# Kernel tuning notes

Measured on AMD Instinct MI355X. Metric: run time of the kernel, lower is better.

The kernel has to match this reference:

```python
import jax, jax.numpy as jnp
import numpy as np

BETA = 1.0
MIN_FEATURE_SIZE = 1.0
NX_RHO, NY_RHO = 32, 32          # control-point grid
NX_PHI, NY_PHI = 480, 240        # level-set evaluation grid (mirrored to 480x480)


def setup_inputs() -> dict:
    key = jax.random.key(0)
    params = jax.random.normal(key, (NX_RHO * NY_RHO,), dtype=jnp.float32)
    x_rho = jnp.linspace(0.0, 1.0, NX_RHO, dtype=jnp.float32)
    y_rho = jnp.linspace(0.0, 1.0, NY_RHO, dtype=jnp.float32)
    x_phi = jnp.linspace(0.0, 1.0, NY_PHI, dtype=jnp.float32)  # len == ny_phi
    y_phi = jnp.linspace(0.0, 1.0, NX_PHI, dtype=jnp.float32)  # len == nx_phi
    return {
        "params": params,
        "x_rho": x_rho, "y_rho": y_rho,
        "x_phi": x_phi, "y_phi": y_phi,
        "nx_phi": NX_PHI, "ny_phi": NY_PHI,
        "rho_size": 1.0 / NX_RHO,      # RBF sigma
        "grid_size": 1.0 / NX_PHI,     # finite-difference spacing
    }


def _points(xv, yv):
    # torch.meshgrid(yv, xv, indexing='ij'); column_stack((first.flat, second.flat))
    Y, X = jnp.meshgrid(yv, xv, indexing="ij")  # [Ny, Nx]
    return jnp.stack([Y.ravel(), X.ravel()], axis=1)  # [Ny*Nx, 2]


def _gauss(pi, pj, sig):
    # exp(-d^2 / (2 sig^2)); skip the sqrt->square round-trip (same forward math)
    d2 = (pi[:, None, 0] - pj[None, :, 0]) ** 2 + (pi[:, None, 1] - pj[None, :, 1]) ** 2
    return jnp.exp(-d2 / (2.0 * sig ** 2))


def _grad1d(phi, d, axis):
    # central diff interior, one-sided at the two borders (matches the torch loop)
    p = jnp.moveaxis(phi, axis, 0)
    g = jnp.concatenate(
        [(p[1:2] - p[0:1]) / d,
         (p[2:] - p[:-2]) / (2.0 * d),
         (p[-1:] - p[-2:-1]) / d], axis=0)
    return jnp.moveaxis(g, 0, axis)


def reference(params, x_rho, y_rho, x_phi, y_phi, nx_phi, ny_phi, rho_size, grid_size):
    # level-set RBF interpolation
    xy0 = _points(x_rho, y_rho)                    # [Nrho, 2]
    K = _gauss(xy0, xy0, rho_size)                 # [Nrho, Nrho]
    model = jnp.linalg.inv(K) @ params             # [Nrho]
    xy1 = _points(x_phi, y_phi)                    # [Nphi, 2]
    phi = _gauss(xy0, xy1, rho_size).T @ model     # [Nphi]
    phi = phi.reshape(nx_phi, ny_phi)
    phi = jnp.concatenate([phi, phi[:, ::-1]], axis=1)  # mirror along y

    SC = 1e-12
    phi_x = _grad1d(phi, grid_size, 0) + SC
    phi_y = _grad1d(phi, grid_size, 1) + SC
    phi_xx = _grad1d(phi_x, grid_size, 0)
    phi_xy = _grad1d(phi_x, grid_size, 1)
    phi_yy = _grad1d(phi_y, grid_size, 1)

    pi_d = np.pi / (1.3 * MIN_FEATURE_SIZE)
    phi_v = jnp.maximum(jnp.sqrt(phi_x ** 2 + phi_y ** 2), 1e-8)
    phi_vv = (phi_x ** 2 * phi_xx + 2.0 * phi_x * phi_y * phi_xy + phi_y ** 2 * phi_yy) / phi_v ** 2
    pen = jnp.maximum(jnp.abs(phi_vv) / (pi_d * jnp.abs(phi) + BETA * phi_v) - pi_d, 0.0)
    return jnp.nansum(pen * grid_size ** 2)
```

## Files before the change

kernel.cpp:

```cpp
#include <hip/hip_runtime.h>
#include <math.h>

#define NR    32
#define NYPHI 240
#define NFULL 480
#define TI    32
#define TJ    16
#define GRID_I (NFULL / TI)
#define GRID_J (NYPHI / TJ)

__global__ __launch_bounds__(256)
void k_all(const float* __restrict__ params,
           const float* __restrict__ x_rho,
           const float* __restrict__ y_rho,
           const float* __restrict__ x_phi,
           const float* __restrict__ y_phi,
           const float* __restrict__ rho_size,
           const float* __restrict__ grid_size,
           float* __restrict__ out)
{
    __shared__ float pb[2][4][NR];
    __shared__ float sRy[NR][NR + 1], sRx[NR][NR + 1];
    __shared__ float sM1[NR][NR + 1], sM [NR][NR + 1];
    __shared__ float sGy[TI + 4][NR + 1];
    __shared__ float sGx[TJ + 4][NR + 1];
    __shared__ float sT [TI + 4][NR + 1];
    __shared__ float sP [TI + 4][TJ + 5];

    const int tid = threadIdx.x;
    const int c   = tid & 31;
    const int w   = tid >> 5;

    const float sig    = rho_size[0];
    const float inv2s2 = 1.0f / (2.0f * sig * sig);
    const float d      = grid_size[0];
    const float invd   = 1.0f / d;
    const float inv2d  = 0.5f * invd;

    const int i0 = blockIdx.y * TI;
    const int j0 = blockIdx.x * TJ;

    float ay[4], ry[4], ax[4], rx[4];
    #pragma unroll
    for (int q = 0; q < 4; ++q) {
        const int r = w + 8 * q;
        const float dy = y_rho[r] - y_rho[c];
        const float dx = x_rho[r] - x_rho[c];
        ay[q] = __expf(-dy * dy * inv2s2);
        ax[q] = __expf(-dx * dx * inv2s2);
        const float id = (r == c) ? 1.0f : 0.0f;
        ry[q] = id;
        rx[q] = id;
    }

    for (int idx = tid; idx < (TI + 4) * NR; idx += 256) {
        const int li = idx >> 5;
        const int a  = idx & 31;
        const int gi = i0 - 2 + li;
        if (gi >= 0 && gi < NFULL) {
            const float dy = y_phi[gi] - y_rho[a];
            sGy[li][a] = __expf(-dy * dy * inv2s2);
        }
        if (li < TJ + 4) {
            const int gj = j0 - 2 + li;
            if (gj >= 0) {
                const int jm = (gj < NYPHI) ? gj : (NFULL - 1 - gj);
                const float dx = x_phi[jm] - x_rho[a];
                sGx[li][a] = __expf(-dx * dx * inv2s2);
            }
        }
    }

    #pragma unroll
    for (int k = 0; k < NR; ++k) {
        const int kw = k & 7, kq = k >> 3, par = k & 1;
        if (w == kw) {
            pb[par][0][c] = ay[kq];
            pb[par][1][c] = ry[kq];
            pb[par][2][c] = ax[kq];
            pb[par][3][c] = rx[kq];
        }
        __syncthreads();
        const float pay = pb[par][0][c], pry = pb[par][1][c];
        const float pax = pb[par][2][c], prx = pb[par][3][c];
        const float iay = __builtin_amdgcn_rcpf(pb[par][0][k]);
        const float iax = __builtin_amdgcn_rcpf(pb[par][2][k]);
        #pragma unroll
        for (int q = 0; q < 4; ++q) {
            const float fy = __shfl(ay[q], k, 32) * iay;
            const float fx = __shfl(ax[q], k, 32) * iax;
            const bool piv = (q == kq) && (w == kw);
            if (!piv) {
                ay[q] -= fy * pay;  ry[q] -= fy * pry;
                ax[q] -= fx * pax;  rx[q] -= fx * prx;
            }
        }
    }

    #pragma unroll
    for (int q = 0; q < 4; ++q) {
        const int r = w + 8 * q;
        const float day = __shfl(ay[q], r, 32);
        const float dax = __shfl(ax[q], r, 32);
        ry[q] *= __builtin_amdgcn_rcpf(day);
        rx[q] *= __builtin_amdgcn_rcpf(dax);
        sRy[r][c] = ry[q];
        sRx[r][c] = rx[q];
    }
    __syncthreads();

    #pragma unroll
    for (int q = 0; q < 4; ++q) {
        const int r = w + 8 * q;
        float s = 0.0f;
        #pragma unroll
        for (int b = 0; b < NR; ++b) s += params[r * NR + b] * sRx[b][c];
        sM1[r][c] = s;
    }
    __syncthreads();

    #pragma unroll
    for (int q = 0; q < 4; ++q) {
        const int r = w + 8 * q;
        float s = 0.0f;
        #pragma unroll
        for (int b = 0; b < NR; ++b) s += sRy[r][b] * sM1[b][c];
        sM[r][c] = s;
    }
    __syncthreads();

    for (int idx = tid; idx < (TI + 4) * NR; idx += 256) {
        const int li = idx >> 5;
        const int b  = idx & 31;
        const int gi = i0 - 2 + li;
        if (gi >= 0 && gi < NFULL) {
            float s = 0.0f;
            #pragma unroll
            for (int a = 0; a < NR; ++a) s += sGy[li][a] * sM[a][b];
            sT[li][b] = s;
        }
    }
    __syncthreads();

    for (int idx = tid; idx < (TI + 4) * (TJ + 4); idx += 256) {
        const int li = idx / (TJ + 4);
        const int lj = idx - li * (TJ + 4);
        const int gi = i0 - 2 + li;
        const int gj = j0 - 2 + lj;
        if (gi >= 0 && gi < NFULL && gj >= 0) {
            float s = 0.0f;
            #pragma unroll
            for (int b = 0; b < NR; ++b) s += sT[li][b] * sGx[lj][b];
            sP[li][lj] = s;
        }
    }
    __syncthreads();

    auto PH = [&](int gi, int gj) -> float {
        return sP[gi - i0 + 2][gj - j0 + 2];
    };
    auto GA = [&](int gi, int gj) -> float {
        if (gi == 0)         return (PH(1, gj)       - PH(0, gj))       * invd;
        if (gi == NFULL - 1) return (PH(NFULL-1, gj) - PH(NFULL-2, gj)) * invd;
        return (PH(gi + 1, gj) - PH(gi - 1, gj)) * inv2d;
    };
    auto GB = [&](int gi, int gj) -> float {
        if (gj == 0)         return (PH(gi, 1)       - PH(gi, 0))       * invd;
        return (PH(gi, gj + 1) - PH(gi, gj - 1)) * inv2d;
    };

    const float SC  = 1e-12f;
    const float pid = (float)(3.14159265358979323846 / 1.3);

    float acc = 0.0f;
    #pragma unroll
    for (int p = 0; p < 2; ++p) {
        const int px_idx = tid + p * 256;
        const int li = px_idx >> 4;
        const int lj = px_idx & 15;
        const int gi = i0 + li;
        const int gj = j0 + lj;

        const float u_c = GA(gi, gj);
        const float v_c = GB(gi, gj);
        const float pxv = u_c + SC;
        const float pyv = v_c + SC;

        float pxx, pxy, pyy;
        if (gi == 0)              pxx = (GA(1, gj) - u_c) * invd;
        else if (gi == NFULL - 1) pxx = (u_c - GA(NFULL - 2, gj)) * invd;
        else                      pxx = (GA(gi + 1, gj) - GA(gi - 1, gj)) * inv2d;

        if (gj == 0)              pxy = (GA(gi, 1) - u_c) * invd;
        else                      pxy = (GA(gi, gj + 1) - GA(gi, gj - 1)) * inv2d;

        if (gj == 0)              pyy = (GB(gi, 1) - v_c) * invd;
        else                      pyy = (GB(gi, gj + 1) - GB(gi, gj - 1)) * inv2d;

        const float phiv  = fmaxf(sqrtf(pxv * pxv + pyv * pyv), 1e-8f);
        const float phivv = (pxv * pxv * pxx + 2.0f * pxv * pyv * pxy + pyv * pyv * pyy)
                            / (phiv * phiv);
        float pen = fmaxf(fabsf(phivv) / (pid * fabsf(PH(gi, gj)) + phiv) - pid, 0.0f);
        if (isnan(pen)) pen = 0.0f;
        acc += pen;
    }

    acc *= 2.0f * d * d;

    #pragma unroll
    for (int o = 32; o > 0; o >>= 1) acc += __shfl_down(acc, o, 64);
    __shared__ float wsum[4];
    const int lane = tid & 63;
    const int wv   = tid >> 6;
    if (lane == 0) wsum[wv] = acc;
    __syncthreads();
    if (tid == 0) {
        const float partial = wsum[0] + wsum[1] + wsum[2] + wsum[3];
        const unsigned POISON = 0xAAAAAAAAu;
        unsigned old = atomicCAS((unsigned*)out, POISON, __float_as_uint(partial));
        if (old != POISON) atomicAdd(out, partial);
    }
}

extern "C" void kernel_launch(void* const* d_in, const int* in_sizes, int n_in,
                              void* d_out, int out_size, void* d_ws, size_t ws_size,
                              hipStream_t stream)
{
    const float* params    = (const float*)d_in[0];
    const float* x_rho     = (const float*)d_in[1];
    const float* y_rho     = (const float*)d_in[2];
    const float* x_phi     = (const float*)d_in[3];
    const float* y_phi     = (const float*)d_in[4];
    const float* rho_size  = (const float*)d_in[7];
    const float* grid_size = (const float*)d_in[8];

    float* out = (float*)d_out;

    hipLaunchKernelGGL(k_all, dim3(GRID_J, GRID_I), dim3(256), 0, stream,
                       params, x_rho, y_rho, x_phi, y_phi,
                       rho_size, grid_size, out);
}
```

Before: 90.85 us.

## Invert RBF kernels in a single wave and overlap with basis setup

Each 32x32 Gaussian matrix is now inverted by one half of a single 64-lane wave, with each lane holding one column in registers and Gauss-Jordan pivots broadcast by shuffles. This removes the 32 block-wide barriers the old elimination needed. The other three waves fill the Gy/Gx basis tiles and stage params into shared memory at the same time. The tile height is halved to 16 so twice as many blocks run with one pixel per thread, and the shared-memory dot products use four partial accumulators. The cost is that the redundant per-block inversion now covers half as many pixels, and a single lane carrying 64 live floats adds register pressure.

```diff
diff --git a/kernel.cpp b/kernel.cpp
--- a/kernel.cpp
+++ b/kernel.cpp
@@ -2,10 +2,13 @@
 #include <math.h>
 
 #define NR    32
+#define NS    36
 #define NYPHI 240
 #define NFULL 480
-#define TI    32
+#define TI    16
 #define TJ    16
+#define HTI   (TI + 4)
+#define HTJ   (TJ + 4)
 #define GRID_I (NFULL / TI)
 #define GRID_J (NYPHI / TJ)
 
@@ -19,18 +22,15 @@
            const float* __restrict__ grid_size,
            float* __restrict__ out)
 {
-    __shared__ float pb[2][4][NR];
-    __shared__ float sRy[NR][NR + 1], sRx[NR][NR + 1];
-    __shared__ float sM1[NR][NR + 1], sM [NR][NR + 1];
-    __shared__ float sGy[TI + 4][NR + 1];
-    __shared__ float sGx[TJ + 4][NR + 1];
-    __shared__ float sT [TI + 4][NR + 1];
-    __shared__ float sP [TI + 4][TJ + 5];
+    __shared__ float sRy[NR][NS], sRx[NR][NS];
+    __shared__ float sPar[NR][NS];
+    __shared__ float sM1[NR][NS], sM[NR][NS];
+    __shared__ float sGy[HTI][NS];
+    __shared__ float sGx[HTJ][NS];
+    __shared__ float sT [HTI][NS];
+    __shared__ float sP [HTI][HTJ + 1];
 
     const int tid = threadIdx.x;
-    const int c   = tid & 31;
-    const int w   = tid >> 5;
-
     const float sig    = rho_size[0];
     const float inv2s2 = 1.0f / (2.0f * sig * sig);
     const float d      = grid_size[0];
@@ -40,28 +40,48 @@
     const int i0 = blockIdx.y * TI;
     const int j0 = blockIdx.x * TJ;
 
-    float ay[4], ry[4], ax[4], rx[4];
-    #pragma unroll
-    for (int q = 0; q < 4; ++q) {
-        const int r = w + 8 * q;
-        const float dy = y_rho[r] - y_rho[c];
-        const float dx = x_rho[r] - x_rho[c];
-        ay[q] = __expf(-dy * dy * inv2s2);
-        ax[q] = __expf(-dx * dx * inv2s2);
-        const float id = (r == c) ? 1.0f : 0.0f;
-        ry[q] = id;
-        rx[q] = id;
-    }
-
-    for (int idx = tid; idx < (TI + 4) * NR; idx += 256) {
-        const int li = idx >> 5;
-        const int a  = idx & 31;
-        const int gi = i0 - 2 + li;
-        if (gi >= 0 && gi < NFULL) {
-            const float dy = y_phi[gi] - y_rho[a];
-            sGy[li][a] = __expf(-dy * dy * inv2s2);
-        }
-        if (li < TJ + 4) {
+    if (tid < 64) {
+        const int sys  = tid >> 5;
+        const int col  = tid & 31;
+        const int ksrc = tid & 32;
+        const float* rho = sys ? x_rho : y_rho;
+        const float rc = rho[col];
+        float A[NR], R[NR];
+        #pragma unroll
+        for (int r = 0; r < NR; ++r) {
+            const float dd = rho[r] - rc;
+            A[r] = __expf(-dd * dd * inv2s2);
+            R[r] = (r == col) ? 1.0f : 0.0f;
+        }
+        #pragma unroll
+        for (int k = 0; k < NR; ++k) {
+            const float piv = __shfl(A[k], ksrc + k, 64);
+            const float pin = __builtin_amdgcn_rcpf(piv);
+            A[k] *= pin;
+            R[k] *= pin;
+            #pragma unroll
+            for (int r = 0; r < NR; ++r) {
+                if (r == k) continue;
+                const float f = __shfl(A[r], ksrc + k, 64);
+                A[r] -= f * A[k];
+                R[r] -= f * R[k];
+            }
+        }
+        #pragma unroll
+        for (int r = 0; r < NR; ++r) {
+            if (sys) sRx[r][col] = R[r];
+            else     sRy[r][col] = R[r];
+        }
+    } else {
+        const int t = tid - 64;
+        for (int idx = t; idx < HTI * NR; idx += 192) {
+            const int li = idx >> 5;
+            const int a  = idx & 31;
+            const int gi = i0 - 2 + li;
+            if (gi >= 0 && gi < NFULL) {
+                const float dy = y_phi[gi] - y_rho[a];
+                sGy[li][a] = __expf(-dy * dy * inv2s2);
+            }
             const int gj = j0 - 2 + li;
             if (gj >= 0) {
                 const int jm = (gj < NYPHI) ? gj : (NFULL - 1 - gj);
@@ -69,89 +89,78 @@
                 sGx[li][a] = __expf(-dx * dx * inv2s2);
             }
         }
-    }
-
-    #pragma unroll
-    for (int k = 0; k < NR; ++k) {
-        const int kw = k & 7, kq = k >> 3, par = k & 1;
-        if (w == kw) {
-            pb[par][0][c] = ay[kq];
-            pb[par][1][c] = ry[kq];
-            pb[par][2][c] = ax[kq];
-            pb[par][3][c] = rx[kq];
-        }
-        __syncthreads();
-        const float pay = pb[par][0][c], pry = pb[par][1][c];
-        const float pax = pb[par][2][c], prx = pb[par][3][c];
-        const float iay = __builtin_amdgcn_rcpf(pb[par][0][k]);
-        const float iax = __builtin_amdgcn_rcpf(pb[par][2][k]);
-        #pragma unroll
-        for (int q = 0; q < 4; ++q) {
-            const float fy = __shfl(ay[q], k, 32) * iay;
-            const float fx = __shfl(ax[q], k, 32) * iax;
-            const bool piv = (q == kq) && (w == kw);
-            if (!piv) {
-                ay[q] -= fy * pay;  ry[q] -= fy * pry;
-                ax[q] -= fx * pax;  rx[q] -= fx * prx;
-            }
-        }
-    }
+        for (int idx = t; idx < NR * NR; idx += 192) {
+            sPar[idx >> 5][idx & 31] = params[idx];
+        }
+    }
+    __syncthreads();
+
+    const int c = tid & 31;
+    const int w = tid >> 5;
 
     #pragma unroll
     for (int q = 0; q < 4; ++q) {
         const int r = w + 8 * q;
-        const float day = __shfl(ay[q], r, 32);
-        const float dax = __shfl(ax[q], r, 32);
-        ry[q] *= __builtin_amdgcn_rcpf(day);
-        rx[q] *= __builtin_amdgcn_rcpf(dax);
-        sRy[r][c] = ry[q];
-        sRx[r][c] = rx[q];
+        float a0 = 0.f, a1 = 0.f, a2 = 0.f, a3 = 0.f;
+        #pragma unroll
+        for (int b = 0; b < NR; b += 4) {
+            a0 += sPar[r][b]     * sRx[b][c];
+            a1 += sPar[r][b + 1] * sRx[b + 1][c];
+            a2 += sPar[r][b + 2] * sRx[b + 2][c];
+            a3 += sPar[r][b + 3] * sRx[b + 3][c];
+        }
+        sM1[r][c] = (a0 + a1) + (a2 + a3);
     }
     __syncthreads();
 
     #pragma unroll
     for (int q = 0; q < 4; ++q) {
         const int r = w + 8 * q;
-        float s = 0.0f;
-        #pragma unroll
-        for (int b = 0; b < NR; ++b) s += params[r * NR + b] * sRx[b][c];
-        sM1[r][c] = s;
-    }
-    __syncthreads();
-
-    #pragma unroll
-    for (int q = 0; q < 4; ++q) {
-        const int r = w + 8 * q;
-        float s = 0.0f;
-        #pragma unroll
-        for (int b = 0; b < NR; ++b) s += sRy[r][b] * sM1[b][c];
-        sM[r][c] = s;
-    }
-    __syncthreads();
-
-    for (int idx = tid; idx < (TI + 4) * NR; idx += 256) {
+        float a0 = 0.f, a1 = 0.f, a2 = 0.f, a3 = 0.f;
+        #pragma unroll
+        for (int b = 0; b < NR; b += 4) {
+            a0 += sRy[r][b]     * sM1[b][c];
+            a1 += sRy[r][b + 1] * sM1[b + 1][c];
+            a2 += sRy[r][b + 2] * sM1[b + 2][c];
+            a3 += sRy[r][b + 3] * sM1[b + 3][c];
+        }
+        sM[r][c] = (a0 + a1) + (a2 + a3);
+    }
+    __syncthreads();
+
+    for (int idx = tid; idx < HTI * NR; idx += 256) {
         const int li = idx >> 5;
         const int b  = idx & 31;
         const int gi = i0 - 2 + li;
         if (gi >= 0 && gi < NFULL) {
-            float s = 0.0f;
+            float a0 = 0.f, a1 = 0.f, a2 = 0.f, a3 = 0.f;
             #pragma unroll
-            for (int a = 0; a < NR; ++a) s += sGy[li][a] * sM[a][b];
-            sT[li][b] = s;
-        }
-    }
-    __syncthreads();
-
-    for (int idx = tid; idx < (TI + 4) * (TJ + 4); idx += 256) {
-        const int li = idx / (TJ + 4);
-        const int lj = idx - li * (TJ + 4);
+            for (int a = 0; a < NR; a += 4) {
+                a0 += sGy[li][a]     * sM[a][b];
+                a1 += sGy[li][a + 1] * sM[a + 1][b];
+                a2 += sGy[li][a + 2] * sM[a + 2][b];
+                a3 += sGy[li][a + 3] * sM[a + 3][b];
+            }
+            sT[li][b] = (a0 + a1) + (a2 + a3);
+        }
+    }
+    __syncthreads();
+
+    for (int idx = tid; idx < HTI * HTJ; idx += 256) {
+        const int li = idx / HTJ;
+        const int lj = idx - li * HTJ;
         const int gi = i0 - 2 + li;
         const int gj = j0 - 2 + lj;
         if (gi >= 0 && gi < NFULL && gj >= 0) {
-            float s = 0.0f;
+            float a0 = 0.f, a1 = 0.f, a2 = 0.f, a3 = 0.f;
             #pragma unroll
-            for (int b = 0; b < NR; ++b) s += sT[li][b] * sGx[lj][b];
-            sP[li][lj] = s;
+            for (int b = 0; b < NR; b += 4) {
+                a0 += sT[li][b]     * sGx[lj][b];
+                a1 += sT[li][b + 1] * sGx[lj][b + 1];
+                a2 += sT[li][b + 2] * sGx[lj][b + 2];
+                a3 += sT[li][b + 3] * sGx[lj][b + 3];
+            }
+            sP[li][lj] = (a0 + a1) + (a2 + a3);
         }
     }
     __syncthreads();
@@ -172,40 +181,34 @@
     const float SC  = 1e-12f;
     const float pid = (float)(3.14159265358979323846 / 1.3);
 
-    float acc = 0.0f;
-    #pragma unroll
-    for (int p = 0; p < 2; ++p) {
-        const int px_idx = tid + p * 256;
-        const int li = px_idx >> 4;
-        const int lj = px_idx & 15;
-        const int gi = i0 + li;
-        const int gj = j0 + lj;
-
-        const float u_c = GA(gi, gj);
-        const float v_c = GB(gi, gj);
-        const float pxv = u_c + SC;
-        const float pyv = v_c + SC;
-
-        float pxx, pxy, pyy;
-        if (gi == 0)              pxx = (GA(1, gj) - u_c) * invd;
-        else if (gi == NFULL - 1) pxx = (u_c - GA(NFULL - 2, gj)) * invd;
-        else                      pxx = (GA(gi + 1, gj) - GA(gi - 1, gj)) * inv2d;
-
-        if (gj == 0)              pxy = (GA(gi, 1) - u_c) * invd;
-        else                      pxy = (GA(gi, gj + 1) - GA(gi, gj - 1)) * inv2d;
-
-        if (gj == 0)              pyy = (GB(gi, 1) - v_c) * invd;
-        else                      pyy = (GB(gi, gj + 1) - GB(gi, gj - 1)) * inv2d;
-
-        const float phiv  = fmaxf(sqrtf(pxv * pxv + pyv * pyv), 1e-8f);
-        const float phivv = (pxv * pxv * pxx + 2.0f * pxv * pyv * pxy + pyv * pyv * pyy)
-                            / (phiv * phiv);
-        float pen = fmaxf(fabsf(phivv) / (pid * fabsf(PH(gi, gj)) + phiv) - pid, 0.0f);
-        if (isnan(pen)) pen = 0.0f;
-        acc += pen;
-    }
-
-    acc *= 2.0f * d * d;
+    const int li = tid >> 4;
+    const int lj = tid & 15;
+    const int gi = i0 + li;
+    const int gj = j0 + lj;
+
+    const float u_c = GA(gi, gj);
+    const float v_c = GB(gi, gj);
+    const float pxv = u_c + SC;
+    const float pyv = v_c + SC;
+
+    float pxx, pxy, pyy;
+    if (gi == 0)              pxx = (GA(1, gj) - u_c) * invd;
+    else if (gi == NFULL - 1) pxx = (u_c - GA(NFULL - 2, gj)) * invd;
+    else                      pxx = (GA(gi + 1, gj) - GA(gi - 1, gj)) * inv2d;
+
+    if (gj == 0)              pxy = (GA(gi, 1) - u_c) * invd;
+    else                      pxy = (GA(gi, gj + 1) - GA(gi, gj - 1)) * inv2d;
+
+    if (gj == 0)              pyy = (GB(gi, 1) - v_c) * invd;
+    else                      pyy = (GB(gi, gj + 1) - GB(gi, gj - 1)) * inv2d;
+
+    const float phiv  = fmaxf(sqrtf(pxv * pxv + pyv * pyv), 1e-8f);
+    const float phivv = (pxv * pxv * pxx + 2.0f * pxv * pyv * pxy + pyv * pyv * pyy)
+                        / (phiv * phiv);
+    float pen = fmaxf(fabsf(phivv) / (pid * fabsf(PH(gi, gj)) + phiv) - pid, 0.0f);
+    if (isnan(pen)) pen = 0.0f;
+
+    float acc = pen * 2.0f * d * d;
 
     #pragma unroll
     for (int o = 32; o > 0; o >>= 1) acc += __shfl_down(acc, o, 64);
```

New measurement: 99.32 us. +9.3%, slower.
